# Kernel optimization log

Hardware: AMD Instinct MI355X
Metric: run time of the kernel (lower is better)

## Reference

```python
import jax, jax.numpy as jnp
import numpy as np


def setup_inputs() -> dict:
    key = jax.random.key(0)
    k1, k2 = jax.random.split(key)
    B, H, N, D = 4, 16, 2048, 64
    x = jax.random.normal(k1, (B, H, N, D), dtype=jnp.float32)
    wqkv = 0.02 * jax.random.normal(k2, (H, D, 3 * D), dtype=jnp.float32)
    bqkv = jnp.zeros((H, 1, 3 * D), dtype=jnp.float32)
    return {"x": x, "wqkv": wqkv, "bqkv": bqkv}


def reference(x, wqkv, bqkv):
    # x: [B, H, N, D]; wqkv: [H, D, 3D]; bqkv: [H, 1, 3D]
    B, H, N, D = x.shape
    scale = D ** (-0.5)
    qkv = jnp.einsum('bhnd,hde->bhne', x, wqkv) + bqkv  # [B,H,N,3D]
    # Faithful to torch: reshape (3D,) -> (D, 3) then unbind last axis,
    # i.e. q/k/v are interleaved (stride-3) columns of the projection.
    qkv = qkv.reshape(B, H, N, D, 3)
    q = qkv[..., 0] * scale
    k = qkv[..., 1]
    v = qkv[..., 2]
    attn = jnp.einsum('bhqd,bhkd->bhqk', q, k)  # [B,H,N,N]
    attn = jax.nn.softmax(attn, axis=-1)
    out = jnp.einsum('bhqk,bhkd->bhqd', attn, v)  # [B,H,N,D]
    return out
```

## Files before the change

kernel.cpp:

```cpp
#include <hip/hip_runtime.h>
#include <hip/hip_bf16.h>
#include <stdint.h>

typedef short bf16x8 __attribute__((ext_vector_type(8)));
typedef short bf16x4 __attribute__((ext_vector_type(4)));
typedef float f32x4 __attribute__((ext_vector_type(4)));

#define BHC 64
#define NQ 2048
#define DD 64
#define NE 192
#define LDP 72
#define QSCALE 0.1803368801111245f

__device__ __forceinline__ short f2bf(float f) {
  unsigned u = __float_as_uint(f);
  unsigned r = (u + 0x7FFFu + ((u >> 16) & 1u)) >> 16;
  return (short)r;
}

__device__ __forceinline__ bf16x8 pack8(float4 a, float4 b) {
  bf16x8 v;
  v[0] = f2bf(a.x); v[1] = f2bf(a.y); v[2] = f2bf(a.z); v[3] = f2bf(a.w);
  v[4] = f2bf(b.x); v[5] = f2bf(b.y); v[6] = f2bf(b.z); v[7] = f2bf(b.w);
  return v;
}

__global__ __launch_bounds__(256, 4) void proj_kernel(
    const float* __restrict__ x, const float* __restrict__ w,
    const float* __restrict__ bq, short* __restrict__ Qg,
    short* __restrict__ Kg, short* __restrict__ Vtg) {
  __shared__ short wt[NE * LDP];
  __shared__ short sV[4][64 * 24];

  const int tid = threadIdx.x;
  const int bh = blockIdx.x >> 5;
  const int rb = blockIdx.x & 31;
  const int h = bh & 15;

  const float* whp = w + (size_t)h * DD * NE;
  for (int i = 0; i < 48; ++i) {
    int idx = i * 256 + tid;
    int d = idx / NE, e = idx - d * NE;
    int dd = e / 3, wh = e - dd * 3;
    wt[(wh * 64 + dd) * LDP + d] = f2bf(whp[idx]);
  }
  __syncthreads();

  const int wave = tid >> 6;
  const int lane = tid & 63;
  const int col = lane & 15, quad = lane >> 4;
  const int row0 = rb * 64 + wave * 16;

  const float* xrow = x + ((size_t)bh * NQ + row0 + col) * DD;
  bf16x8 aq[2];
#pragma unroll
  for (int kc = 0; kc < 2; ++kc) {
    const float4* p4 = (const float4*)(xrow + kc * 32 + quad * 8);
    aq[kc] = pack8(p4[0], p4[1]);
  }

  f32x4 acc[12];
#pragma unroll
  for (int nt = 0; nt < 12; ++nt) acc[nt] = (f32x4){0.f, 0.f, 0.f, 0.f};

#pragma unroll
  for (int nt = 0; nt < 12; ++nt) {
#pragma unroll
    for (int kc = 0; kc < 2; ++kc) {
      bf16x8 bw = *(const bf16x8*)(&wt[(nt * 16 + col) * LDP + kc * 32 + quad * 8]);
      acc[nt] = __builtin_amdgcn_mfma_f32_16x16x32_bf16(aq[kc], bw, acc[nt], 0, 0, 0);
    }
  }

  const float* bqh = bq + h * NE;
  short* Qp = Qg + ((size_t)bh * NQ + row0) * DD;
  short* Kp = Kg + ((size_t)bh * NQ + row0) * DD;
  short* sVw = sV[wave];

#pragma unroll
  for (int nt = 0; nt < 12; ++nt) {
    int rho = nt * 16 + col;
    float bias = bqh[(rho & 63) * 3 + (rho >> 6)];
#pragma unroll
    for (int r = 0; r < 4; ++r) {
      float val = acc[nt][r] + bias;
      int rowl = quad * 4 + r;
      if (nt < 4) {
        Qp[rowl * DD + nt * 16 + col] = f2bf(val * QSCALE);
      } else if (nt < 8) {
        Kp[rowl * DD + (nt - 4) * 16 + col] = f2bf(val);
      } else {
        sVw[((nt - 8) * 16 + col) * 24 + rowl] = f2bf(val);
      }
    }
  }

  short* Vp = Vtg + (size_t)bh * DD * NQ + row0;
#pragma unroll
  for (int c = 0; c < 2; ++c) {
    int idx = c * 64 + lane;
    int d = idx >> 1, half = (idx & 1) * 8;
    *(bf16x8*)(Vp + (size_t)d * NQ + half) = *(const bf16x8*)(sVw + d * 24 + half);
  }
}

__global__ __launch_bounds__(256, 2) void attn_kernel(
    const short* __restrict__ Qg, const short* __restrict__ Kg,
    const short* __restrict__ Vtg, float* __restrict__ out) {
  __shared__ short kbuf[2][64 * LDP];
  __shared__ short vbuf[2][64 * LDP];
  __shared__ short pbuf[4][64 * LDP];

  const int tid = threadIdx.x;
  const int bh = blockIdx.x >> 3;
  const int qb = blockIdx.x & 7;
  const int wave = tid >> 6, lane = tid & 63;
  const int col = lane & 15, quad = lane >> 4;
  const int qbase = qb * 256 + wave * 64;

  bf16x8 bqf[4][2];
#pragma unroll
  for (int ntq = 0; ntq < 4; ++ntq)
#pragma unroll
    for (int kc = 0; kc < 2; ++kc)
      bqf[ntq][kc] = *(const bf16x8*)(Qg + ((size_t)bh * NQ + qbase + ntq * 16 + col) * DD +
                                      kc * 32 + quad * 8);

  f32x4 o[4][4];
  float l_acc[4];
#pragma unroll
  for (int mtq = 0; mtq < 4; ++mtq) {
    l_acc[mtq] = 0.f;
#pragma unroll
    for (int ntd = 0; ntd < 4; ++ntd) o[mtq][ntd] = (f32x4){0.f, 0.f, 0.f, 0.f};
  }

  short* pb = pbuf[wave];
  const short* Kb = Kg + (size_t)bh * NQ * DD;
  const short* Vb = Vtg + (size_t)bh * DD * NQ;

  const int sr0 = tid >> 3, so0 = (tid & 7) * 8;
  const int sr1 = (256 + tid) >> 3, so1 = ((256 + tid) & 7) * 8;

  {
    bf16x8 k0 = *(const bf16x8*)(Kb + sr0 * DD + so0);
    bf16x8 k1 = *(const bf16x8*)(Kb + sr1 * DD + so1);
    bf16x8 v0 = *(const bf16x8*)(Vb + (size_t)sr0 * NQ + so0);
    bf16x8 v1 = *(const bf16x8*)(Vb + (size_t)sr1 * NQ + so1);
    *(bf16x8*)(&kbuf[0][sr0 * LDP + so0]) = k0;
    *(bf16x8*)(&kbuf[0][sr1 * LDP + so1]) = k1;
    *(bf16x8*)(&vbuf[0][sr0 * LDP + so0]) = v0;
    *(bf16x8*)(&vbuf[0][sr1 * LDP + so1]) = v1;
  }
  __syncthreads();

#pragma unroll 1
  for (int t = 0; t < 32; ++t) {
    const int p = t & 1;
    const short* kb = kbuf[p];
    const short* vb_s = vbuf[p];

    bf16x8 nk0, nk1, nv0, nv1;
    if (t < 31) {
      const short* Kn = Kb + (t + 1) * 64 * DD;
      const short* Vn = Vb + (t + 1) * 64;
      nk0 = *(const bf16x8*)(Kn + sr0 * DD + so0);
      nk1 = *(const bf16x8*)(Kn + sr1 * DD + so1);
      nv0 = *(const bf16x8*)(Vn + (size_t)sr0 * NQ + so0);
      nv1 = *(const bf16x8*)(Vn + (size_t)sr1 * NQ + so1);
    }

#pragma unroll
    for (int mtk = 0; mtk < 4; ++mtk) {
      bf16x8 ka0 = *(const bf16x8*)(&kb[(mtk * 16 + col) * LDP + quad * 8]);
      bf16x8 ka1 = *(const bf16x8*)(&kb[(mtk * 16 + col) * LDP + 32 + quad * 8]);
#pragma unroll
      for (int ntq = 0; ntq < 4; ++ntq) {
        f32x4 s = (f32x4){0.f, 0.f, 0.f, 0.f};
        s = __builtin_amdgcn_mfma_f32_16x16x32_bf16(ka0, bqf[ntq][0], s, 0, 0, 0);
        s = __builtin_amdgcn_mfma_f32_16x16x32_bf16(ka1, bqf[ntq][1], s, 0, 0, 0);
        float p0 = __builtin_amdgcn_exp2f(s[0]);
        float p1 = __builtin_amdgcn_exp2f(s[1]);
        float p2 = __builtin_amdgcn_exp2f(s[2]);
        float p3 = __builtin_amdgcn_exp2f(s[3]);
        l_acc[ntq] += (p0 + p1) + (p2 + p3);
        bf16x4 pv;
        pv[0] = f2bf(p0); pv[1] = f2bf(p1); pv[2] = f2bf(p2); pv[3] = f2bf(p3);
        *(bf16x4*)(&pb[(ntq * 16 + col) * LDP + mtk * 16 + quad * 4]) = pv;
      }
    }

    bf16x8 vf[4][2];
#pragma unroll
    for (int ntd = 0; ntd < 4; ++ntd)
#pragma unroll
      for (int kc = 0; kc < 2; ++kc)
        vf[ntd][kc] = *(const bf16x8*)(&vb_s[(ntd * 16 + col) * LDP + kc * 32 + quad * 8]);

#pragma unroll
    for (int mtq = 0; mtq < 4; ++mtq) {
      bf16x8 ap0 = *(const bf16x8*)(&pb[(mtq * 16 + col) * LDP + quad * 8]);
      bf16x8 ap1 = *(const bf16x8*)(&pb[(mtq * 16 + col) * LDP + 32 + quad * 8]);
#pragma unroll
      for (int ntd = 0; ntd < 4; ++ntd) {
        o[mtq][ntd] = __builtin_amdgcn_mfma_f32_16x16x32_bf16(ap0, vf[ntd][0], o[mtq][ntd], 0, 0, 0);
        o[mtq][ntd] = __builtin_amdgcn_mfma_f32_16x16x32_bf16(ap1, vf[ntd][1], o[mtq][ntd], 0, 0, 0);
      }
    }

    if (t < 31) {
      short* kn = kbuf[1 - p];
      short* vn = vbuf[1 - p];
      *(bf16x8*)(&kn[sr0 * LDP + so0]) = nk0;
      *(bf16x8*)(&kn[sr1 * LDP + so1]) = nk1;
      *(bf16x8*)(&vn[sr0 * LDP + so0]) = nv0;
      *(bf16x8*)(&vn[sr1 * LDP + so1]) = nv1;
      __syncthreads();
    }
  }

#pragma unroll
  for (int mtq = 0; mtq < 4; ++mtq) {
    float l = l_acc[mtq];
    l += __shfl_xor(l, 16);
    l += __shfl_xor(l, 32);
#pragma unroll
    for (int r = 0; r < 4; ++r) {
      float inv = 1.0f / __shfl(l, quad * 4 + r);
      int rq = qbase + mtq * 16 + quad * 4 + r;
      float* orow = out + ((size_t)bh * NQ + rq) * DD;
#pragma unroll
      for (int ntd = 0; ntd < 4; ++ntd) orow[ntd * 16 + col] = o[mtq][ntd][r] * inv;
    }
  }
}

extern "C" void kernel_launch(void* const* d_in, const int* in_sizes, int n_in,
                              void* d_out, int out_size, void* d_ws, size_t ws_size,
                              hipStream_t stream) {
  const float* x = (const float*)d_in[0];
  const float* w = (const float*)d_in[1];
  const float* bq = (const float*)d_in[2];
  float* out = (float*)d_out;

  short* Qg = (short*)d_ws;
  short* Kg = Qg + (size_t)BHC * NQ * DD;
  short* Vtg = Kg + (size_t)BHC * NQ * DD;

  proj_kernel<<<dim3(2048), dim3(256), 0, stream>>>(x, w, bq, Qg, Kg, Vtg);
  attn_kernel<<<dim3(512), dim3(256), 0, stream>>>(Qg, Kg, Vtg, out);
}
```

Measured before the change: 185.1 us.

## Swizzle K/V shared tiles, split P into halves, compute row sums via MFMA

The attention kernel now stores K/V tiles in XOR-swizzled unpadded shared memory and processes the 64-key tile in two 32-key halves, which shrinks the P buffer. Softmax row sums are accumulated by an extra MFMA against a ones vector instead of scalar adds and cross-lane shuffles. Block-to-(bh,qb) mapping is transposed, and bf16 conversion uses the packed hardware intrinsic in both kernels. The projection kernel pads the weight tile per q/k/v slice. The aim is fewer bank conflicts, less VALU work and lower LDS use, at the cost of extra MFMA work and a row sum taken from bf16-rounded P.

```diff
diff --git a/kernel.cpp b/kernel.cpp
--- a/kernel.cpp
+++ b/kernel.cpp
@@ -11,6 +11,8 @@
 #define DD 64
 #define NE 192
 #define LDP 72
+#define WPS (64 * LDP + 8)
+#define PLP 36
 #define QSCALE 0.1803368801111245f
 
 __device__ __forceinline__ short f2bf(float f) {
@@ -26,11 +28,16 @@
   return v;
 }
 
+__device__ __forceinline__ short2 pk_bf16(float a, float b) {
+  __hip_bfloat162 c = __float22bfloat162_rn(make_float2(a, b));
+  return *reinterpret_cast<short2*>(&c);
+}
+
 __global__ __launch_bounds__(256, 4) void proj_kernel(
     const float* __restrict__ x, const float* __restrict__ w,
     const float* __restrict__ bq, short* __restrict__ Qg,
     short* __restrict__ Kg, short* __restrict__ Vtg) {
-  __shared__ short wt[NE * LDP];
+  __shared__ short wt[3 * WPS];
   __shared__ short sV[4][64 * 24];
 
   const int tid = threadIdx.x;
@@ -43,7 +50,7 @@
     int idx = i * 256 + tid;
     int d = idx / NE, e = idx - d * NE;
     int dd = e / 3, wh = e - dd * 3;
-    wt[(wh * 64 + dd) * LDP + d] = f2bf(whp[idx]);
+    wt[wh * WPS + dd * LDP + d] = f2bf(whp[idx]);
   }
   __syncthreads();
 
@@ -66,9 +73,10 @@
 
 #pragma unroll
   for (int nt = 0; nt < 12; ++nt) {
+    const short* wrow = &wt[(nt >> 2) * WPS + ((nt & 3) * 16 + col) * LDP];
 #pragma unroll
     for (int kc = 0; kc < 2; ++kc) {
-      bf16x8 bw = *(const bf16x8*)(&wt[(nt * 16 + col) * LDP + kc * 32 + quad * 8]);
+      bf16x8 bw = *(const bf16x8*)(wrow + kc * 32 + quad * 8);
       acc[nt] = __builtin_amdgcn_mfma_f32_16x16x32_bf16(aq[kc], bw, acc[nt], 0, 0, 0);
     }
   }
@@ -80,19 +88,23 @@
 
 #pragma unroll
   for (int nt = 0; nt < 12; ++nt) {
-    int rho = nt * 16 + col;
-    float bias = bqh[(rho & 63) * 3 + (rho >> 6)];
-#pragma unroll
-    for (int r = 0; r < 4; ++r) {
-      float val = acc[nt][r] + bias;
-      int rowl = quad * 4 + r;
-      if (nt < 4) {
-        Qp[rowl * DD + nt * 16 + col] = f2bf(val * QSCALE);
-      } else if (nt < 8) {
-        Kp[rowl * DD + (nt - 4) * 16 + col] = f2bf(val);
-      } else {
-        sVw[((nt - 8) * 16 + col) * 24 + rowl] = f2bf(val);
-      }
+    int dd = (nt & 3) * 16 + col;
+    float bias = bqh[dd * 3 + (nt >> 2)];
+    float v0 = acc[nt][0] + bias, v1 = acc[nt][1] + bias;
+    float v2 = acc[nt][2] + bias, v3 = acc[nt][3] + bias;
+    if (nt < 4) { v0 *= QSCALE; v1 *= QSCALE; v2 *= QSCALE; v3 *= QSCALE; }
+    short2 s01 = pk_bf16(v0, v1);
+    short2 s23 = pk_bf16(v2, v3);
+    int rowl = quad * 4;
+    if (nt < 4) {
+      Qp[rowl * DD + dd] = s01.x; Qp[(rowl + 1) * DD + dd] = s01.y;
+      Qp[(rowl + 2) * DD + dd] = s23.x; Qp[(rowl + 3) * DD + dd] = s23.y;
+    } else if (nt < 8) {
+      Kp[rowl * DD + dd] = s01.x; Kp[(rowl + 1) * DD + dd] = s01.y;
+      Kp[(rowl + 2) * DD + dd] = s23.x; Kp[(rowl + 3) * DD + dd] = s23.y;
+    } else {
+      sVw[dd * 24 + rowl] = s01.x; sVw[dd * 24 + rowl + 1] = s01.y;
+      sVw[dd * 24 + rowl + 2] = s23.x; sVw[dd * 24 + rowl + 3] = s23.y;
     }
   }
 
@@ -108,13 +120,13 @@
 __global__ __launch_bounds__(256, 2) void attn_kernel(
     const short* __restrict__ Qg, const short* __restrict__ Kg,
     const short* __restrict__ Vtg, float* __restrict__ out) {
-  __shared__ short kbuf[2][64 * LDP];
-  __shared__ short vbuf[2][64 * LDP];
-  __shared__ short pbuf[4][64 * LDP];
+  __shared__ short kbuf[2][64 * 64];
+  __shared__ short vbuf[2][64 * 64];
+  __shared__ short pbuf[4][64 * PLP];
 
   const int tid = threadIdx.x;
-  const int bh = blockIdx.x >> 3;
-  const int qb = blockIdx.x & 7;
+  const int bh = blockIdx.x & 63;
+  const int qb = blockIdx.x >> 6;
   const int wave = tid >> 6, lane = tid & 63;
   const int col = lane & 15, quad = lane >> 4;
   const int qbase = qb * 256 + wave * 64;
@@ -127,11 +139,15 @@
       bqf[ntq][kc] = *(const bf16x8*)(Qg + ((size_t)bh * NQ + qbase + ntq * 16 + col) * DD +
                                       kc * 32 + quad * 8);
 
+  bf16x8 onesf;
+#pragma unroll
+  for (int j = 0; j < 8; ++j) onesf[j] = (short)0x3F80;
+
   f32x4 o[4][4];
-  float l_acc[4];
+  f32x4 l4[4];
 #pragma unroll
   for (int mtq = 0; mtq < 4; ++mtq) {
-    l_acc[mtq] = 0.f;
+    l4[mtq] = (f32x4){0.f, 0.f, 0.f, 0.f};
 #pragma unroll
     for (int ntd = 0; ntd < 4; ++ntd) o[mtq][ntd] = (f32x4){0.f, 0.f, 0.f, 0.f};
   }
@@ -140,18 +156,22 @@
   const short* Kb = Kg + (size_t)bh * NQ * DD;
   const short* Vb = Vtg + (size_t)bh * DD * NQ;
 
-  const int sr0 = tid >> 3, so0 = (tid & 7) * 8;
-  const int sr1 = (256 + tid) >> 3, so1 = ((256 + tid) & 7) * 8;
+  const int r0 = tid >> 3, c0 = tid & 7;
+  const int dst0 = r0 * 64 + ((c0 ^ (r0 & 7)) * 8);
+  const int dst1 = (r0 + 32) * 64 + ((c0 ^ (r0 & 7)) * 8);
+  const int src0 = r0 * DD + c0 * 8;
+  const size_t vsrc0o = (size_t)r0 * NQ + c0 * 8;
+  const size_t vsrc1o = (size_t)(r0 + 32) * NQ + c0 * 8;
 
   {
-    bf16x8 k0 = *(const bf16x8*)(Kb + sr0 * DD + so0);
-    bf16x8 k1 = *(const bf16x8*)(Kb + sr1 * DD + so1);
-    bf16x8 v0 = *(const bf16x8*)(Vb + (size_t)sr0 * NQ + so0);
-    bf16x8 v1 = *(const bf16x8*)(Vb + (size_t)sr1 * NQ + so1);
-    *(bf16x8*)(&kbuf[0][sr0 * LDP + so0]) = k0;
-    *(bf16x8*)(&kbuf[0][sr1 * LDP + so1]) = k1;
-    *(bf16x8*)(&vbuf[0][sr0 * LDP + so0]) = v0;
-    *(bf16x8*)(&vbuf[0][sr1 * LDP + so1]) = v1;
+    bf16x8 k0 = *(const bf16x8*)(Kb + src0);
+    bf16x8 k1 = *(const bf16x8*)(Kb + src0 + 32 * DD);
+    bf16x8 v0 = *(const bf16x8*)(Vb + vsrc0o);
+    bf16x8 v1 = *(const bf16x8*)(Vb + vsrc1o);
+    *(bf16x8*)(&kbuf[0][dst0]) = k0;
+    *(bf16x8*)(&kbuf[0][dst1]) = k1;
+    *(bf16x8*)(&vbuf[0][dst0]) = v0;
+    *(bf16x8*)(&vbuf[0][dst1]) = v1;
   }
   __syncthreads();
 
@@ -165,69 +185,65 @@
     if (t < 31) {
       const short* Kn = Kb + (t + 1) * 64 * DD;
       const short* Vn = Vb + (t + 1) * 64;
-      nk0 = *(const bf16x8*)(Kn + sr0 * DD + so0);
-      nk1 = *(const bf16x8*)(Kn + sr1 * DD + so1);
-      nv0 = *(const bf16x8*)(Vn + (size_t)sr0 * NQ + so0);
-      nv1 = *(const bf16x8*)(Vn + (size_t)sr1 * NQ + so1);
-    }
-
-#pragma unroll
-    for (int mtk = 0; mtk < 4; ++mtk) {
-      bf16x8 ka0 = *(const bf16x8*)(&kb[(mtk * 16 + col) * LDP + quad * 8]);
-      bf16x8 ka1 = *(const bf16x8*)(&kb[(mtk * 16 + col) * LDP + 32 + quad * 8]);
-#pragma unroll
-      for (int ntq = 0; ntq < 4; ++ntq) {
-        f32x4 s = (f32x4){0.f, 0.f, 0.f, 0.f};
-        s = __builtin_amdgcn_mfma_f32_16x16x32_bf16(ka0, bqf[ntq][0], s, 0, 0, 0);
-        s = __builtin_amdgcn_mfma_f32_16x16x32_bf16(ka1, bqf[ntq][1], s, 0, 0, 0);
-        float p0 = __builtin_amdgcn_exp2f(s[0]);
-        float p1 = __builtin_amdgcn_exp2f(s[1]);
-        float p2 = __builtin_amdgcn_exp2f(s[2]);
-        float p3 = __builtin_amdgcn_exp2f(s[3]);
-        l_acc[ntq] += (p0 + p1) + (p2 + p3);
-        bf16x4 pv;
-        pv[0] = f2bf(p0); pv[1] = f2bf(p1); pv[2] = f2bf(p2); pv[3] = f2bf(p3);
-        *(bf16x4*)(&pb[(ntq * 16 + col) * LDP + mtk * 16 + quad * 4]) = pv;
+      nk0 = *(const bf16x8*)(Kn + src0);
+      nk1 = *(const bf16x8*)(Kn + src0 + 32 * DD);
+      nv0 = *(const bf16x8*)(Vn + vsrc0o);
+      nv1 = *(const bf16x8*)(Vn + vsrc1o);
+    }
+
+#pragma unroll
+    for (int h = 0; h < 2; ++h) {
+#pragma unroll
+      for (int j = 0; j < 2; ++j) {
+        const int krow = (2 * h + j) * 16 + col;
+        const int kx = krow & 7;
+        bf16x8 ka0 = *(const bf16x8*)(&kb[krow * 64 + ((quad ^ kx) * 8)]);
+        bf16x8 ka1 = *(const bf16x8*)(&kb[krow * 64 + (((4 + quad) ^ kx) * 8)]);
+#pragma unroll
+        for (int ntq = 0; ntq < 4; ++ntq) {
+          f32x4 s = (f32x4){0.f, 0.f, 0.f, 0.f};
+          s = __builtin_amdgcn_mfma_f32_16x16x32_bf16(ka0, bqf[ntq][0], s, 0, 0, 0);
+          s = __builtin_amdgcn_mfma_f32_16x16x32_bf16(ka1, bqf[ntq][1], s, 0, 0, 0);
+          float p0 = __builtin_amdgcn_exp2f(s[0]);
+          float p1 = __builtin_amdgcn_exp2f(s[1]);
+          float p2 = __builtin_amdgcn_exp2f(s[2]);
+          float p3 = __builtin_amdgcn_exp2f(s[3]);
+          short2 s01 = pk_bf16(p0, p1);
+          short2 s23 = pk_bf16(p2, p3);
+          bf16x4 pv; pv[0] = s01.x; pv[1] = s01.y; pv[2] = s23.x; pv[3] = s23.y;
+          *(bf16x4*)(&pb[(ntq * 16 + col) * PLP + j * 16 + quad * 4]) = pv;
+        }
       }
-    }
-
-    bf16x8 vf[4][2];
-#pragma unroll
-    for (int ntd = 0; ntd < 4; ++ntd)
-#pragma unroll
-      for (int kc = 0; kc < 2; ++kc)
-        vf[ntd][kc] = *(const bf16x8*)(&vb_s[(ntd * 16 + col) * LDP + kc * 32 + quad * 8]);
-
-#pragma unroll
-    for (int mtq = 0; mtq < 4; ++mtq) {
-      bf16x8 ap0 = *(const bf16x8*)(&pb[(mtq * 16 + col) * LDP + quad * 8]);
-      bf16x8 ap1 = *(const bf16x8*)(&pb[(mtq * 16 + col) * LDP + 32 + quad * 8]);
-#pragma unroll
-      for (int ntd = 0; ntd < 4; ++ntd) {
-        o[mtq][ntd] = __builtin_amdgcn_mfma_f32_16x16x32_bf16(ap0, vf[ntd][0], o[mtq][ntd], 0, 0, 0);
-        o[mtq][ntd] = __builtin_amdgcn_mfma_f32_16x16x32_bf16(ap1, vf[ntd][1], o[mtq][ntd], 0, 0, 0);
+
+#pragma unroll
+      for (int mtq = 0; mtq < 4; ++mtq) {
+        bf16x8 ap = *(const bf16x8*)(&pb[(mtq * 16 + col) * PLP + quad * 8]);
+#pragma unroll
+        for (int ntd = 0; ntd < 4; ++ntd) {
+          const int vrow = ntd * 16 + col;
+          bf16x8 vf = *(const bf16x8*)(&vb_s[vrow * 64 + (((h * 4 + quad) ^ (vrow & 7)) * 8)]);
+          o[mtq][ntd] = __builtin_amdgcn_mfma_f32_16x16x32_bf16(ap, vf, o[mtq][ntd], 0, 0, 0);
+        }
+        l4[mtq] = __builtin_amdgcn_mfma_f32_16x16x32_bf16(ap, onesf, l4[mtq], 0, 0, 0);
       }
     }
 
     if (t < 31) {
       short* kn = kbuf[1 - p];
       short* vn = vbuf[1 - p];
-      *(bf16x8*)(&kn[sr0 * LDP + so0]) = nk0;
-      *(bf16x8*)(&kn[sr1 * LDP + so1]) = nk1;
-      *(bf16x8*)(&vn[sr0 * LDP + so0]) = nv0;
-      *(bf16x8*)(&vn[sr1 * LDP + so1]) = nv1;
+      *(bf16x8*)(&kn[dst0]) = nk0;
+      *(bf16x8*)(&kn[dst1]) = nk1;
+      *(bf16x8*)(&vn[dst0]) = nv0;
+      *(bf16x8*)(&vn[dst1]) = nv1;
       __syncthreads();
     }
   }
 
 #pragma unroll
   for (int mtq = 0; mtq < 4; ++mtq) {
-    float l = l_acc[mtq];
-    l += __shfl_xor(l, 16);
-    l += __shfl_xor(l, 32);
 #pragma unroll
     for (int r = 0; r < 4; ++r) {
-      float inv = 1.0f / __shfl(l, quad * 4 + r);
+      float inv = 1.0f / l4[mtq][r];
       int rq = qbase + mtq * 16 + quad * 4 + r;
       float* orow = out + ((size_t)bh * NQ + rq) * DD;
 #pragma unroll
```

After: 203.4 us. +9.9%, slower.
